# Kernel tuning notes

Hardware: AMD Instinct MI355X
Metric: run time of the kernel (lower is better)

## Reference

```python
import jax, jax.numpy as jnp
import numpy as np

N_DIM = 144           # 9 * patch_size(16)
NUM_CODES = 50257


def setup_inputs() -> dict:
    key = jax.random.key(0)
    k1, k2 = jax.random.split(key)
    z = jax.random.normal(k1, (4, 1024, N_DIM), dtype=jnp.float32)
    # embedding initialized uniform(-1/K, 1/K) as in the torch module
    emb = jax.random.uniform(k2, (NUM_CODES, N_DIM), dtype=jnp.float32,
                             minval=-1.0 / NUM_CODES, maxval=1.0 / NUM_CODES)
    return {"z": z, "emb": emb, "pkeep": 0}


def reference(z, emb, pkeep):
    # flatten to [N, D]
    zf = z.reshape(-1, N_DIM)
    # squared euclidean distances: ||z||^2 + ||e||^2 - 2 z e^T  -> [N, K]
    d = (jnp.sum(zf * zf, axis=1, keepdims=True)
         + jnp.sum(emb * emb, axis=1)
         - 2.0 * jnp.matmul(zf, emb.T))
    min_encoding_indices = jnp.argmin(d, axis=1)          # [N] int
    z_q = emb[min_encoding_indices].reshape(z.shape)      # gather + reshape
    loss = jnp.mean((z_q - z) ** 2)
    # pkeep == 0 in this configuration -> random-replacement branch skipped
    return (z_q, min_encoding_indices, loss)
```

## Files before the change

kernel.cpp:

```cpp
#include <hip/hip_runtime.h>
#include <math.h>

#define D        144
#define KCODES   50257
#define NROWS    4096
#define NS       16
#define CHUNK    3142
#define NT       50
#define NTSW     52
#define CAP      512
#define MARGIN   6.0e-5f
#define ZQ_OFF   0
#define IDX_OFF  589824
#define LOSS_OFF 593920

typedef short bf16x8 __attribute__((ext_vector_type(8)));
typedef float f32x4  __attribute__((ext_vector_type(4)));

#define EHSW_SZ  ((size_t)NS * NTSW * 4 * 5 * 64 * 16)
#define CNT_OFF  EHSW_SZ
#define RMX_OFF  (CNT_OFF + (size_t)NROWS * 4)
#define LIST_OFF (RMX_OFF + (size_t)NROWS * 4)
#define LROW_OFF (LIST_OFF + (size_t)NROWS * CAP * 4)
#define WS_NEED  (LROW_OFF + (size_t)NROWS * 4)

static __device__ __forceinline__ unsigned short f2bf(float x) {
    unsigned int u = __float_as_uint(x);
    u += 0x7fffu + ((u >> 16) & 1u);
    return (unsigned short)(u >> 16);
}
static __device__ __forceinline__ unsigned fkey(float f) {
    unsigned u = __float_as_uint(f);
    return (u & 0x80000000u) ? ~u : (u | 0x80000000u);
}
static __device__ __forceinline__ float fkey_inv(unsigned k) {
    unsigned u = (k & 0x80000000u) ? (k ^ 0x80000000u) : ~k;
    return __uint_as_float(u);
}

__global__ void prep_emb_kernel(const float* __restrict__ emb,
                                unsigned short* __restrict__ EHsw,
                                int* __restrict__ cnt, unsigned* __restrict__ rmx) {
    const int idx = blockIdx.x * 256 + threadIdx.x;
    if (idx < NROWS) { cnt[idx] = 0; rmx[idx] = 0u; }
    if (idx >= NS * NTSW * 4 * 5 * 64) return;
    const int lane = idx & 63;
    int r = idx >> 6;
    const int ks = r % 5;  r /= 5;
    const int w  = r % 4;  r /= 4;
    const int t  = r % NTSW;
    const int sp = r / NTSW;
    const int n  = lane & 15, q = lane >> 4;
    const int code = sp * CHUNK + t * 64 + w * 16 + n;
    const int k0   = ks * 32 + q * 8;
    unsigned short h[8];
    if (code < KCODES && k0 < D) {
        const float4 f0 = *(const float4*)(emb + (size_t)code * D + k0);
        const float4 f1 = *(const float4*)(emb + (size_t)code * D + k0 + 4);
        const float f[8] = {f0.x, f0.y, f0.z, f0.w, f1.x, f1.y, f1.z, f1.w};
        #pragma unroll
        for (int j = 0; j < 8; ++j) h[j] = f2bf(f[j]);
    } else {
        #pragma unroll
        for (int j = 0; j < 8; ++j) h[j] = 0;
    }
    *(uint4*)(EHsw + (size_t)idx * 8) = *(const uint4*)h;
}

#define LOAD_A_FRAGS(zptr)                                                     \
    bf16x8 Ah[4][5];                                                           \
    _Pragma("unroll")                                                          \
    for (int rt = 0; rt < 4; ++rt) {                                           \
        const float* zr = (zptr) + (size_t)(row0 + rt * 16 + n) * D;           \
        _Pragma("unroll")                                                      \
        for (int ks = 0; ks < 5; ++ks) {                                       \
            const int k0 = ks * 32 + q * 8;                                    \
            bf16x8 h;                                                          \
            if (k0 < D) {                                                      \
                const float4 f0 = *(const float4*)(zr + k0);                   \
                const float4 f1 = *(const float4*)(zr + k0 + 4);               \
                const float f[8] = {f0.x, f0.y, f0.z, f0.w,                    \
                                    f1.x, f1.y, f1.z, f1.w};                   \
                _Pragma("unroll")                                              \
                for (int j = 0; j < 8; ++j) h[j] = (short)f2bf(f[j]);          \
            } else {                                                           \
                _Pragma("unroll")                                              \
                for (int j = 0; j < 8; ++j) h[j] = 0;                          \
            }                                                                  \
            Ah[rt][ks] = h;                                                    \
        }                                                                      \
    }

#define LOAD_B(buf, ptr)                                                       \
    _Pragma("unroll")                                                          \
    for (int ks = 0; ks < 5; ++ks)                                             \
        buf[ks] = *(const bf16x8*)((ptr) + (size_t)ks * 1024);

#define MFMA_TILE(buf)                                                         \
    _Pragma("unroll")                                                          \
    for (int rt = 0; rt < 4; ++rt) {                                           \
        acc[rt][0]=0.f; acc[rt][1]=0.f; acc[rt][2]=0.f; acc[rt][3]=0.f;        \
    }                                                                          \
    _Pragma("unroll")                                                          \
    for (int ks = 0; ks < 5; ++ks)                                             \
        _Pragma("unroll")                                                      \
        for (int rt = 0; rt < 4; ++rt)                                         \
            acc[rt] = __builtin_amdgcn_mfma_f32_16x16x32_bf16(                 \
                Ah[rt][ks], buf[ks], acc[rt], 0, 0, 0);

#define CONSUME_MAX                                                            \
    _Pragma("unroll")                                                          \
    for (int rt = 0; rt < 4; ++rt)                                             \
        _Pragma("unroll")                                                      \
        for (int r = 0; r < 4; ++r)                                            \
            ml[rt*4 + r] = fmaxf(ml[rt*4 + r], acc[rt][r]);

#define CONSUME_SEL                                                            \
    _Pragma("unroll")                                                          \
    for (int rt = 0; rt < 4; ++rt)                                             \
        _Pragma("unroll")                                                      \
        for (int r = 0; r < 4; ++r) {                                          \
            const float vm = 2.0f * acc[rt][r];                                \
            if (vm >= thr[rt*4 + r] && code < KCODES) {                        \
                const int row = row0 + rt * 16 + q * 4 + r;                    \
                const int pos = atomicAdd(&cnt[row], 1);                       \
                if (pos < CAP) list[(size_t)row * CAP + pos] = code;           \
            }                                                                  \
        }                                                                      \
    code += 64;

#define TS 20480

__global__ __launch_bounds__(256, 2)
void vq_max_kernel(const float* __restrict__ z,
                   const char* __restrict__ EHsw,
                   unsigned* __restrict__ rmx) {
    const int tid  = threadIdx.x;
    const int w    = tid >> 6;
    const int lane = tid & 63;
    const int n    = lane & 15;
    const int q    = lane >> 4;
    const int sp   = blockIdx.x;
    const int row0 = blockIdx.y * 64;

    LOAD_A_FRAGS(z)

    float ml[16];
    #pragma unroll
    for (int i = 0; i < 16; ++i) ml[i] = -INFINITY;

    const char* pB = EHsw + ((size_t)(sp * NTSW) * 4 + w) * 5120 + lane * 16;

    bf16x8 b0[5], b1[5], b2[5], b3[5];
    f32x4 acc[4];
    LOAD_B(b0, pB)
    LOAD_B(b1, pB + TS)
    LOAD_B(b2, pB + 2 * TS)
    LOAD_B(b3, pB + 3 * TS)
    for (int i = 0; i < 12; ++i) {
        MFMA_TILE(b0) CONSUME_MAX LOAD_B(b0, pB + 4 * TS)
        MFMA_TILE(b1) CONSUME_MAX LOAD_B(b1, pB + 5 * TS)
        MFMA_TILE(b2) CONSUME_MAX LOAD_B(b2, pB + 6 * TS)
        MFMA_TILE(b3) CONSUME_MAX LOAD_B(b3, pB + 7 * TS)
        pB += 4 * TS;
    }
    MFMA_TILE(b0) CONSUME_MAX
    MFMA_TILE(b1) CONSUME_MAX

    __shared__ float wmax[4][64];
    #pragma unroll
    for (int i = 0; i < 16; ++i) {
        float v = ml[i];
        v = fmaxf(v, __shfl_xor(v, 1, 64));
        v = fmaxf(v, __shfl_xor(v, 2, 64));
        v = fmaxf(v, __shfl_xor(v, 4, 64));
        v = fmaxf(v, __shfl_xor(v, 8, 64));
        if (n == 0) wmax[w][(i >> 2) * 16 + q * 4 + (i & 3)] = v;
    }
    __syncthreads();
    if (tid < 64) {
        const float m = fmaxf(fmaxf(wmax[0][tid], wmax[1][tid]),
                              fmaxf(wmax[2][tid], wmax[3][tid])) * 2.0f;
        atomicMax(&rmx[row0 + tid], fkey(m));
    }
}

__global__ __launch_bounds__(256, 2)
void vq_select_kernel(const float* __restrict__ z,
                      const char* __restrict__ EHsw,
                      const unsigned* __restrict__ rmx,
                      int* __restrict__ cnt, int* __restrict__ list) {
    const int tid  = threadIdx.x;
    const int w    = tid >> 6;
    const int lane = tid & 63;
    const int n    = lane & 15;
    const int q    = lane >> 4;
    const int sp   = blockIdx.x;
    const int row0 = blockIdx.y * 64;

    LOAD_A_FRAGS(z)

    float thr[16];
    #pragma unroll
    for (int i = 0; i < 16; ++i) {
        const int row = row0 + (i >> 2) * 16 + q * 4 + (i & 3);
        thr[i] = fkey_inv(rmx[row]) - MARGIN;
    }

    const char* pB = EHsw + ((size_t)(sp * NTSW) * 4 + w) * 5120 + lane * 16;
    int code = sp * CHUNK + w * 16 + n;

    bf16x8 b0[5], b1[5], b2[5], b3[5];
    f32x4 acc[4];
    LOAD_B(b0, pB)
    LOAD_B(b1, pB + TS)
    LOAD_B(b2, pB + 2 * TS)
    LOAD_B(b3, pB + 3 * TS)
    for (int i = 0; i < 12; ++i) {
        MFMA_TILE(b0) CONSUME_SEL LOAD_B(b0, pB + 4 * TS)
        MFMA_TILE(b1) CONSUME_SEL LOAD_B(b1, pB + 5 * TS)
        MFMA_TILE(b2) CONSUME_SEL LOAD_B(b2, pB + 6 * TS)
        MFMA_TILE(b3) CONSUME_SEL LOAD_B(b3, pB + 7 * TS)
        pB += 4 * TS;
    }
    MFMA_TILE(b0) CONSUME_SEL
    MFMA_TILE(b1) CONSUME_SEL
}

__global__ void vq_phaseC_kernel(const float* __restrict__ z,
                                 const float* __restrict__ emb,
                                 const int* __restrict__ cnt,
                                 const int* __restrict__ list,
                                 float* __restrict__ out,
                                 float* __restrict__ lrow) {
    const int r   = blockIdx.x;
    const int tid = threadIdx.x;
    const int lane = tid & 63, wid = tid >> 6;
    __shared__ float zs[D];
    __shared__ float As_;
    __shared__ float bd_s[4]; __shared__ int bi_s[4];
    __shared__ int   bc_s;
    __shared__ float ls_s[4];

    if (tid < D) zs[tid] = z[(size_t)r * D + tid];
    __syncthreads();
    if (tid == 0) {
        float s = 0.f;
        for (int k = 0; k < D; ++k) s = fmaf(zs[k], zs[k], s);
        As_ = s;
    }
    __syncthreads();
    const float A = As_;

    const int nc   = cnt[r];
    const bool full = (nc <= 0) || (nc > CAP);
    const int count = full ? KCODES : nc;

    float bd = INFINITY; int bi = 0x7fffffff;
    for (int i = tid; i < count; i += 256) {
        const int c = full ? i : list[(size_t)r * CAP + i];
        const float4* e4 = (const float4*)(emb + (size_t)c * D);
        float acc = 0.f;
        #pragma unroll
        for (int j = 0; j < 36; ++j) {
            const float4 e = e4[j];
            acc = fmaf(zs[4*j],   e.x, acc);
            acc = fmaf(zs[4*j+1], e.y, acc);
            acc = fmaf(zs[4*j+2], e.z, acc);
            acc = fmaf(zs[4*j+3], e.w, acc);
        }
        const float m2 = 2.0f * acc;
        const float d  = A - m2;
        if (d < bd || (d == bd && c < bi)) { bd = d; bi = c; }
    }
    #pragma unroll
    for (int m = 1; m < 64; m <<= 1) {
        const float od = __shfl_xor(bd, m, 64);
        const int   oi = __shfl_xor(bi, m, 64);
        if (od < bd || (od == bd && oi < bi)) { bd = od; bi = oi; }
    }
    if (lane == 0) { bd_s[wid] = bd; bi_s[wid] = bi; }
    __syncthreads();
    if (tid == 0) {
        float fbd = bd_s[0]; int fbi = bi_s[0];
        for (int k = 1; k < 4; ++k) {
            if (bd_s[k] < fbd || (bd_s[k] == fbd && bi_s[k] < fbi)) { fbd = bd_s[k]; fbi = bi_s[k]; }
        }
        bc_s = fbi;
        out[IDX_OFF + r] = (float)fbi;
    }
    __syncthreads();
    const int bc = bc_s;

    float ls = 0.f;
    if (tid < D) {
        const float e = emb[(size_t)bc * D + tid];
        out[(size_t)r * D + tid] = e;
        const float dl = e - zs[tid];
        ls = dl * dl;
    }
    #pragma unroll
    for (int m = 1; m < 64; m <<= 1) ls += __shfl_xor(ls, m, 64);
    if (lane == 0) ls_s[wid] = ls;
    __syncthreads();
    if (tid == 0) lrow[r] = ls_s[0] + ls_s[1] + ls_s[2] + ls_s[3];
}

__global__ void vq_loss_kernel(const float* __restrict__ lrow, float* __restrict__ out) {
    __shared__ float sm[256];
    const int tid = threadIdx.x;
    float s = 0.f;
    for (int i = tid; i < NROWS; i += 256) s += lrow[i];
    sm[tid] = s; __syncthreads();
    for (int st = 128; st > 0; st >>= 1) {
        if (tid < st) sm[tid] += sm[tid + st];
        __syncthreads();
    }
    if (tid == 0) out[LOSS_OFF] = sm[0] / 589824.0f;
}

#define BM 64
#define BN 64
#define LDP 68
__global__ __launch_bounds__(256, 2)
void vq_argmin_fb(const float* __restrict__ z, const float* __restrict__ emb,
                  float* __restrict__ pd, int* __restrict__ pi) {
    __shared__ float zsm[D][LDP];
    __shared__ float esm[D][LDP];
    __shared__ float Asm[BM];
    const int tid = threadIdx.x;
    const int row0 = blockIdx.x * BM;
    const int sp = blockIdx.y;
    const int c0 = sp * CHUNK;
    const int c1 = (c0 + CHUNK < KCODES) ? (c0 + CHUNK) : KCODES;
    {
        const int r = tid >> 2, p = tid & 3;
        const float4* src = (const float4*)(z + (size_t)(row0 + r) * D);
        #pragma unroll
        for (int i = 0; i < 9; ++i) {
            const int j4 = p + 4 * i;
            const float4 v = src[j4];
            zsm[4*j4+0][r] = v.x; zsm[4*j4+1][r] = v.y;
            zsm[4*j4+2][r] = v.z; zsm[4*j4+3][r] = v.w;
        }
    }
    __syncthreads();
    if (tid < BM) {
        float s = 0.f;
        for (int k = 0; k < D; ++k) { const float t = zsm[k][tid]; s = fmaf(t, t, s); }
        Asm[tid] = s;
    }
    __syncthreads();
    const int tx = tid & 15, ty = tid >> 4;
    float Arow[4];
    #pragma unroll
    for (int i = 0; i < 4; ++i) Arow[i] = Asm[ty*4 + i];
    float bestd[4]; int besti[4];
    #pragma unroll
    for (int i = 0; i < 4; ++i) { bestd[i] = INFINITY; besti[i] = 0x7fffffff; }
    const int ntiles = (c1 - c0 + BN - 1) / BN;
    for (int t = 0; t < ntiles; ++t) {
        const int cb = c0 + t * BN;
        __syncthreads();
        {
            const int cl = tid >> 2, p = tid & 3;
            int crow = cb + cl; if (crow >= KCODES) crow = KCODES - 1;
            const float4* src = (const float4*)(emb + (size_t)crow * D);
            #pragma unroll
            for (int i = 0; i < 9; ++i) {
                const int j4 = p + 4 * i;
                const float4 v = src[j4];
                esm[4*j4+0][cl] = v.x; esm[4*j4+1][cl] = v.y;
                esm[4*j4+2][cl] = v.z; esm[4*j4+3][cl] = v.w;
            }
        }
        __syncthreads();
        float acc[4][4];
        #pragma unroll
        for (int i = 0; i < 4; ++i)
            #pragma unroll
            for (int j = 0; j < 4; ++j) acc[i][j] = 0.f;
        #pragma unroll 4
        for (int k = 0; k < D; ++k) {
            const float4 a = *(const float4*)&zsm[k][ty*4];
            const float4 b = *(const float4*)&esm[k][tx*4];
            acc[0][0]=fmaf(a.x,b.x,acc[0][0]); acc[0][1]=fmaf(a.x,b.y,acc[0][1]);
            acc[0][2]=fmaf(a.x,b.z,acc[0][2]); acc[0][3]=fmaf(a.x,b.w,acc[0][3]);
            acc[1][0]=fmaf(a.y,b.x,acc[1][0]); acc[1][1]=fmaf(a.y,b.y,acc[1][1]);
            acc[1][2]=fmaf(a.y,b.z,acc[1][2]); acc[1][3]=fmaf(a.y,b.w,acc[1][3]);
            acc[2][0]=fmaf(a.z,b.x,acc[2][0]); acc[2][1]=fmaf(a.z,b.y,acc[2][1]);
            acc[2][2]=fmaf(a.z,b.z,acc[2][2]); acc[2][3]=fmaf(a.z,b.w,acc[2][3]);
            acc[3][0]=fmaf(a.w,b.x,acc[3][0]); acc[3][1]=fmaf(a.w,b.y,acc[3][1]);
            acc[3][2]=fmaf(a.w,b.z,acc[3][2]); acc[3][3]=fmaf(a.w,b.w,acc[3][3]);
        }
        #pragma unroll
        for (int j = 0; j < 4; ++j) {
            const int code = cb + tx*4 + j;
            if (code < c1) {
                #pragma unroll
                for (int i = 0; i < 4; ++i) {
                    const float m2 = 2.0f * acc[i][j];
                    const float d  = Arow[i] - m2;
                    if (d < bestd[i] || (d == bestd[i] && code < besti[i])) {
                        bestd[i] = d; besti[i] = code;
                    }
                }
            }
        }
    }
    #pragma unroll
    for (int i = 0; i < 4; ++i) {
        float d = bestd[i]; int idx = besti[i];
        #pragma unroll
        for (int m = 1; m < 16; m <<= 1) {
            const float od = __shfl_xor(d, m, 64);
            const int   oi = __shfl_xor(idx, m, 64);
            if (od < d || (od == d && oi < idx)) { d = od; idx = oi; }
        }
        if (tx == 0) {
            const int r = row0 + ty*4 + i;
            pd[(size_t)sp * NROWS + r] = d;
            pi[(size_t)sp * NROWS + r] = idx;
        }
    }
}

__global__ void vq_finalize_fb(const float* __restrict__ z, const float* __restrict__ emb,
                               const float* __restrict__ pd, const int* __restrict__ pi,
                               float* __restrict__ out, float* __restrict__ lrow) {
    const int r = blockIdx.x * blockDim.x + threadIdx.x;
    if (r >= NROWS) return;
    float bd = INFINITY; int bi = 0x7fffffff;
    for (int s = 0; s < NS; ++s) {
        const float d = pd[(size_t)s * NROWS + r];
        const int  ix = pi[(size_t)s * NROWS + r];
        if (d < bd || (d == bd && ix < bi)) { bd = d; bi = ix; }
    }
    out[IDX_OFF + r] = (float)bi;
    const float4* e4 = (const float4*)(emb + (size_t)bi * D);
    const float4* z4 = (const float4*)(z + (size_t)r * D);
    float4* o4 = (float4*)(out + (size_t)r * D);
    float ls = 0.f;
    #pragma unroll
    for (int j = 0; j < 36; ++j) {
        const float4 e = e4[j], zz = z4[j];
        o4[j] = e;
        const float dx = e.x - zz.x, dy = e.y - zz.y;
        const float dz_ = e.z - zz.z, dw = e.w - zz.w;
        ls += dx*dx + dy*dy + dz_*dz_ + dw*dw;
    }
    lrow[r] = ls;
}

extern "C" void kernel_launch(void* const* d_in, const int* in_sizes, int n_in,
                              void* d_out, int out_size, void* d_ws, size_t ws_size,
                              hipStream_t stream) {
    const float* z   = (const float*)d_in[0];
    const float* emb = (const float*)d_in[1];
    float* out = (float*)d_out;

    if (ws_size >= WS_NEED) {
        unsigned short* EHsw = (unsigned short*)d_ws;
        int*      cnt  = (int*)((char*)d_ws + CNT_OFF);
        unsigned* rmx  = (unsigned*)((char*)d_ws + RMX_OFF);
        int*      list = (int*)((char*)d_ws + LIST_OFF);
        float*    lrow = (float*)((char*)d_ws + LROW_OFF);

        prep_emb_kernel<<<(NS * NTSW * 4 * 5 * 64) / 256, 256, 0, stream>>>(emb, EHsw, cnt, rmx);
        dim3 gs(NS, 64);
        vq_max_kernel<<<gs, 256, 0, stream>>>(z, (const char*)EHsw, rmx);
        vq_select_kernel<<<gs, 256, 0, stream>>>(z, (const char*)EHsw, rmx, cnt, list);
        vq_phaseC_kernel<<<NROWS, 256, 0, stream>>>(z, emb, cnt, list, out, lrow);
        vq_loss_kernel<<<1, 256, 0, stream>>>(lrow, out);
    } else {
        float* pd   = (float*)d_ws;
        int*   pi   = (int*)((char*)d_ws + (size_t)NS * NROWS * 4);
        float* lrow = (float*)((char*)d_ws + (size_t)NS * NROWS * 8);
        dim3 g1(64, NS);
        vq_argmin_fb<<<g1, 256, 0, stream>>>(z, emb, pd, pi);
        vq_finalize_fb<<<16, 256, 0, stream>>>(z, emb, pd, pi, out, lrow);
        vq_loss_kernel<<<1, 256, 0, stream>>>(lrow, out);
    }
}
```

Measured before the change: 282.4 us.

## Double code splits, pre-swizzle z to bf16, warp-skip selection, per-warp exact rescoring

Splits the codebook into 32 chunks instead of 16, giving twice as many blocks for the max and select passes. A new prep kernel converts z to bf16 in MFMA fragment order once, so those passes no longer re-convert z in every block. The select pass now checks all candidates per wave with __any before issuing atomics, and compares against a pre-halved threshold. The exact rescoring kernel assigns one candidate per wave, reduces with shuffles, and computes the norm with a warp reduction. The cost is an extra kernel launch and more per-block prologue work relative to the shorter inner loop.

Result: slower. 427.4 us (+51.4%).

```diff
diff --git a/kernel.cpp b/kernel.cpp
--- a/kernel.cpp
+++ b/kernel.cpp
@@ -4,21 +4,24 @@
 #define D        144
 #define KCODES   50257
 #define NROWS    4096
-#define NS       16
-#define CHUNK    3142
-#define NT       50
-#define NTSW     52
+#define NS       32
+#define CHUNK    1571
+#define NT       25
+#define NTSW     29
 #define CAP      512
 #define MARGIN   6.0e-5f
 #define ZQ_OFF   0
 #define IDX_OFF  589824
 #define LOSS_OFF 593920
+#define TS       20480
 
 typedef short bf16x8 __attribute__((ext_vector_type(8)));
 typedef float f32x4  __attribute__((ext_vector_type(4)));
 
-#define EHSW_SZ  ((size_t)NS * NTSW * 4 * 5 * 64 * 16)
-#define CNT_OFF  EHSW_SZ
+#define EHSW_SZ  ((size_t)NS * NTSW * TS)
+#define ZSW_OFF  EHSW_SZ
+#define ZSW_SZ   ((size_t)64 * 4 * 5 * 64 * 16)
+#define CNT_OFF  (ZSW_OFF + ZSW_SZ)
 #define RMX_OFF  (CNT_OFF + (size_t)NROWS * 4)
 #define LIST_OFF (RMX_OFF + (size_t)NROWS * 4)
 #define LROW_OFF (LIST_OFF + (size_t)NROWS * CAP * 4)
@@ -39,11 +42,8 @@
 }
 
 __global__ void prep_emb_kernel(const float* __restrict__ emb,
-                                unsigned short* __restrict__ EHsw,
-                                int* __restrict__ cnt, unsigned* __restrict__ rmx) {
+                                unsigned short* __restrict__ EHsw) {
     const int idx = blockIdx.x * 256 + threadIdx.x;
-    if (idx < NROWS) { cnt[idx] = 0; rmx[idx] = 0u; }
-    if (idx >= NS * NTSW * 4 * 5 * 64) return;
     const int lane = idx & 63;
     int r = idx >> 6;
     const int ks = r % 5;  r /= 5;
@@ -67,29 +67,41 @@
     *(uint4*)(EHsw + (size_t)idx * 8) = *(const uint4*)h;
 }
 
-#define LOAD_A_FRAGS(zptr)                                                     \
+__global__ void prep_z_kernel(const float* __restrict__ z,
+                              unsigned short* __restrict__ ZSW,
+                              int* __restrict__ cnt, unsigned* __restrict__ rmx) {
+    const int idx = blockIdx.x * 256 + threadIdx.x;
+    if (idx < NROWS) { cnt[idx] = 0; rmx[idx] = 0u; }
+    const int lane = idx & 63;
+    int r = idx >> 6;
+    const int ks = r % 5;  r /= 5;
+    const int rt = r % 4;
+    const int rb = r / 4;
+    const int n  = lane & 15, q = lane >> 4;
+    const int row = rb * 64 + rt * 16 + n;
+    const int k0  = ks * 32 + q * 8;
+    unsigned short h[8];
+    if (k0 < D) {
+        const float4 f0 = *(const float4*)(z + (size_t)row * D + k0);
+        const float4 f1 = *(const float4*)(z + (size_t)row * D + k0 + 4);
+        const float f[8] = {f0.x, f0.y, f0.z, f0.w, f1.x, f1.y, f1.z, f1.w};
+        #pragma unroll
+        for (int j = 0; j < 8; ++j) h[j] = f2bf(f[j]);
+    } else {
+        #pragma unroll
+        for (int j = 0; j < 8; ++j) h[j] = 0;
+    }
+    *(uint4*)(ZSW + (size_t)idx * 8) = *(const uint4*)h;
+}
+
+#define LOAD_A_SW(zsw)                                                         \
     bf16x8 Ah[4][5];                                                           \
     _Pragma("unroll")                                                          \
-    for (int rt = 0; rt < 4; ++rt) {                                           \
-        const float* zr = (zptr) + (size_t)(row0 + rt * 16 + n) * D;           \
+    for (int rt = 0; rt < 4; ++rt)                                             \
         _Pragma("unroll")                                                      \
-        for (int ks = 0; ks < 5; ++ks) {                                       \
-            const int k0 = ks * 32 + q * 8;                                    \
-            bf16x8 h;                                                          \
-            if (k0 < D) {                                                      \
-                const float4 f0 = *(const float4*)(zr + k0);                   \
-                const float4 f1 = *(const float4*)(zr + k0 + 4);               \
-                const float f[8] = {f0.x, f0.y, f0.z, f0.w,                    \
-                                    f1.x, f1.y, f1.z, f1.w};                   \
-                _Pragma("unroll")                                              \
-                for (int j = 0; j < 8; ++j) h[j] = (short)f2bf(f[j]);          \
-            } else {                                                           \
-                _Pragma("unroll")                                              \
-                for (int j = 0; j < 8; ++j) h[j] = 0;                          \
-            }                                                                  \
-            Ah[rt][ks] = h;                                                    \
-        }                                                                      \
-    }
+        for (int ks = 0; ks < 5; ++ks)                                         \
+            Ah[rt][ks] = *(const bf16x8*)((zsw) +                              \
+                (size_t)((((rb * 4 + rt) * 5 + ks) * 64 + lane)) * 16);
 
 #define LOAD_B(buf, ptr)                                                       \
     _Pragma("unroll")                                                          \
@@ -116,23 +128,29 @@
             ml[rt*4 + r] = fmaxf(ml[rt*4 + r], acc[rt][r]);
 
 #define CONSUME_SEL                                                            \
-    _Pragma("unroll")                                                          \
-    for (int rt = 0; rt < 4; ++rt)                                             \
+    {                                                                          \
+        bool anyl = false;                                                     \
         _Pragma("unroll")                                                      \
-        for (int r = 0; r < 4; ++r) {                                          \
-            const float vm = 2.0f * acc[rt][r];                                \
-            if (vm >= thr[rt*4 + r] && code < KCODES) {                        \
-                const int row = row0 + rt * 16 + q * 4 + r;                    \
-                const int pos = atomicAdd(&cnt[row], 1);                       \
-                if (pos < CAP) list[(size_t)row * CAP + pos] = code;           \
-            }                                                                  \
+        for (int rt = 0; rt < 4; ++rt)                                         \
+            _Pragma("unroll")                                                  \
+            for (int r = 0; r < 4; ++r)                                        \
+                anyl |= (acc[rt][r] >= thr2[rt*4 + r]);                        \
+        if (__any(anyl)) {                                                     \
+            _Pragma("unroll")                                                  \
+            for (int rt = 0; rt < 4; ++rt)                                     \
+                _Pragma("unroll")                                              \
+                for (int r = 0; r < 4; ++r)                                    \
+                    if (acc[rt][r] >= thr2[rt*4 + r] && code < KCODES) {       \
+                        const int row = row0 + rt * 16 + q * 4 + r;            \
+                        const int pos = atomicAdd(&cnt[row], 1);               \
+                        if (pos < CAP) list[(size_t)row * CAP + pos] = code;   \
+                    }                                                          \
         }                                                                      \
-    code += 64;
-
-#define TS 20480
+        code += 64;                                                            \
+    }
 
 __global__ __launch_bounds__(256, 2)
-void vq_max_kernel(const float* __restrict__ z,
+void vq_max_kernel(const char* __restrict__ ZSW,
                    const char* __restrict__ EHsw,
                    unsigned* __restrict__ rmx) {
     const int tid  = threadIdx.x;
@@ -141,9 +159,10 @@
     const int n    = lane & 15;
     const int q    = lane >> 4;
     const int sp   = blockIdx.x;
-    const int row0 = blockIdx.y * 64;
-
-    LOAD_A_FRAGS(z)
+    const int rb   = blockIdx.y;
+    const int row0 = rb * 64;
+
+    LOAD_A_SW(ZSW)
 
     float ml[16];
     #pragma unroll
@@ -157,7 +176,7 @@
     LOAD_B(b1, pB + TS)
     LOAD_B(b2, pB + 2 * TS)
     LOAD_B(b3, pB + 3 * TS)
-    for (int i = 0; i < 12; ++i) {
+    for (int i = 0; i < 6; ++i) {
         MFMA_TILE(b0) CONSUME_MAX LOAD_B(b0, pB + 4 * TS)
         MFMA_TILE(b1) CONSUME_MAX LOAD_B(b1, pB + 5 * TS)
         MFMA_TILE(b2) CONSUME_MAX LOAD_B(b2, pB + 6 * TS)
@@ -165,7 +184,6 @@
         pB += 4 * TS;
     }
     MFMA_TILE(b0) CONSUME_MAX
-    MFMA_TILE(b1) CONSUME_MAX
 
     __shared__ float wmax[4][64];
     #pragma unroll
@@ -186,7 +204,7 @@
 }
 
 __global__ __launch_bounds__(256, 2)
-void vq_select_kernel(const float* __restrict__ z,
+void vq_select_kernel(const char* __restrict__ ZSW,
                       const char* __restrict__ EHsw,
                       const unsigned* __restrict__ rmx,
                       int* __restrict__ cnt, int* __restrict__ list) {
@@ -196,15 +214,16 @@
     const int n    = lane & 15;
     const int q    = lane >> 4;
     const int sp   = blockIdx.x;
-    const int row0 = blockIdx.y * 64;
-
-    LOAD_A_FRAGS(z)
-
-    float thr[16];
+    const int rb   = blockIdx.y;
+    const int row0 = rb * 64;
+
+    LOAD_A_SW(ZSW)
+
+    float thr2[16];
     #pragma unroll
     for (int i = 0; i < 16; ++i) {
         const int row = row0 + (i >> 2) * 16 + q * 4 + (i & 3);
-        thr[i] = fkey_inv(rmx[row]) - MARGIN;
+        thr2[i] = (fkey_inv(rmx[row]) - MARGIN) * 0.5f;
     }
 
     const char* pB = EHsw + ((size_t)(sp * NTSW) * 4 + w) * 5120 + lane * 16;
@@ -216,7 +235,7 @@
     LOAD_B(b1, pB + TS)
     LOAD_B(b2, pB + 2 * TS)
     LOAD_B(b3, pB + 3 * TS)
-    for (int i = 0; i < 12; ++i) {
+    for (int i = 0; i < 6; ++i) {
         MFMA_TILE(b0) CONSUME_SEL LOAD_B(b0, pB + 4 * TS)
         MFMA_TILE(b1) CONSUME_SEL LOAD_B(b1, pB + 5 * TS)
         MFMA_TILE(b2) CONSUME_SEL LOAD_B(b2, pB + 6 * TS)
@@ -224,7 +243,6 @@
         pB += 4 * TS;
     }
     MFMA_TILE(b0) CONSUME_SEL
-    MFMA_TILE(b1) CONSUME_SEL
 }
 
 __global__ void vq_phaseC_kernel(const float* __restrict__ z,
@@ -233,77 +251,64 @@
                                  const int* __restrict__ list,
                                  float* __restrict__ out,
                                  float* __restrict__ lrow) {
-    const int r   = blockIdx.x;
-    const int tid = threadIdx.x;
+    const int r    = blockIdx.x;
+    const int tid  = threadIdx.x;
     const int lane = tid & 63, wid = tid >> 6;
-    __shared__ float zs[D];
-    __shared__ float As_;
+    __shared__ float4 zs4[36];
     __shared__ float bd_s[4]; __shared__ int bi_s[4];
     __shared__ int   bc_s;
-    __shared__ float ls_s[4];
-
-    if (tid < D) zs[tid] = z[(size_t)r * D + tid];
-    __syncthreads();
-    if (tid == 0) {
-        float s = 0.f;
-        for (int k = 0; k < D; ++k) s = fmaf(zs[k], zs[k], s);
-        As_ = s;
-    }
-    __syncthreads();
-    const float A = As_;
+
+    if (tid < 36) zs4[tid] = ((const float4*)(z + (size_t)r * D))[tid];
+    __syncthreads();
+
+    float4 z4 = {0.f, 0.f, 0.f, 0.f};
+    if (lane < 36) z4 = zs4[lane];
+
+    float a = z4.x*z4.x + z4.y*z4.y + z4.z*z4.z + z4.w*z4.w;
+    #pragma unroll
+    for (int m = 1; m < 64; m <<= 1) a += __shfl_xor(a, m, 64);
+    const float A = a;
 
     const int nc   = cnt[r];
     const bool full = (nc <= 0) || (nc > CAP);
     const int count = full ? KCODES : nc;
 
     float bd = INFINITY; int bi = 0x7fffffff;
-    for (int i = tid; i < count; i += 256) {
-        const int c = full ? i : list[(size_t)r * CAP + i];
-        const float4* e4 = (const float4*)(emb + (size_t)c * D);
-        float acc = 0.f;
-        #pragma unroll
-        for (int j = 0; j < 36; ++j) {
-            const float4 e = e4[j];
-            acc = fmaf(zs[4*j],   e.x, acc);
-            acc = fmaf(zs[4*j+1], e.y, acc);
-            acc = fmaf(zs[4*j+2], e.z, acc);
-            acc = fmaf(zs[4*j+3], e.w, acc);
-        }
-        const float m2 = 2.0f * acc;
-        const float d  = A - m2;
+    for (int ci = wid; ci < count; ci += 4) {
+        const int c = full ? ci : list[(size_t)r * CAP + ci];
+        float4 e4 = {0.f, 0.f, 0.f, 0.f};
+        if (lane < 36) e4 = ((const float4*)(emb + (size_t)c * D))[lane];
+        float p = z4.x*e4.x + z4.y*e4.y + z4.z*e4.z + z4.w*e4.w;
+        #pragma unroll
+        for (int m = 1; m < 64; m <<= 1) p += __shfl_xor(p, m, 64);
+        const float d = A - 2.0f * p;
         if (d < bd || (d == bd && c < bi)) { bd = d; bi = c; }
-    }
-    #pragma unroll
-    for (int m = 1; m < 64; m <<= 1) {
-        const float od = __shfl_xor(bd, m, 64);
-        const int   oi = __shfl_xor(bi, m, 64);
-        if (od < bd || (od == bd && oi < bi)) { bd = od; bi = oi; }
     }
     if (lane == 0) { bd_s[wid] = bd; bi_s[wid] = bi; }
     __syncthreads();
     if (tid == 0) {
         float fbd = bd_s[0]; int fbi = bi_s[0];
-        for (int k = 1; k < 4; ++k) {
+        for (int k = 1; k < 4; ++k)
             if (bd_s[k] < fbd || (bd_s[k] == fbd && bi_s[k] < fbi)) { fbd = bd_s[k]; fbi = bi_s[k]; }
-        }
         bc_s = fbi;
         out[IDX_OFF + r] = (float)fbi;
     }
     __syncthreads();
     const int bc = bc_s;
 
-    float ls = 0.f;
-    if (tid < D) {
-        const float e = emb[(size_t)bc * D + tid];
-        out[(size_t)r * D + tid] = e;
-        const float dl = e - zs[tid];
-        ls = dl * dl;
-    }
-    #pragma unroll
-    for (int m = 1; m < 64; m <<= 1) ls += __shfl_xor(ls, m, 64);
-    if (lane == 0) ls_s[wid] = ls;
-    __syncthreads();
-    if (tid == 0) lrow[r] = ls_s[0] + ls_s[1] + ls_s[2] + ls_s[3];
+    if (wid == 0) {
+        float ls = 0.f;
+        if (lane < 36) {
+            const float4 e4 = ((const float4*)(emb + (size_t)bc * D))[lane];
+            ((float4*)(out + (size_t)r * D))[lane] = e4;
+            const float dx = e4.x - z4.x, dy = e4.y - z4.y;
+            const float dz_ = e4.z - z4.z, dw = e4.w - z4.w;
+            ls = dx*dx + dy*dy + dz_*dz_ + dw*dw;
+        }
+        #pragma unroll
+        for (int m = 1; m < 64; m <<= 1) ls += __shfl_xor(ls, m, 64);
+        if (lane == 0) lrow[r] = ls;
+    }
 }
 
 __global__ void vq_loss_kernel(const float* __restrict__ lrow, float* __restrict__ out) {
@@ -319,6 +324,7 @@
     if (tid == 0) out[LOSS_OFF] = sm[0] / 589824.0f;
 }
 
+#define FCHUNK 3142
 #define BM 64
 #define BN 64
 #define LDP 68
@@ -331,8 +337,8 @@
     const int tid = threadIdx.x;
     const int row0 = blockIdx.x * BM;
     const int sp = blockIdx.y;
-    const int c0 = sp * CHUNK;
-    const int c1 = (c0 + CHUNK < KCODES) ? (c0 + CHUNK) : KCODES;
+    const int c0 = sp * FCHUNK;
+    const int c1 = (c0 + FCHUNK < KCODES) ? (c0 + FCHUNK) : KCODES;
     {
         const int r = tid >> 2, p = tid & 3;
         const float4* src = (const float4*)(z + (size_t)(row0 + r) * D);
@@ -431,7 +437,7 @@
     const int r = blockIdx.x * blockDim.x + threadIdx.x;
     if (r >= NROWS) return;
     float bd = INFINITY; int bi = 0x7fffffff;
-    for (int s = 0; s < NS; ++s) {
+    for (int s = 0; s < 16; ++s) {
         const float d = pd[(size_t)s * NROWS + r];
         const int  ix = pi[(size_t)s * NROWS + r];
         if (d < bd || (d == bd && ix < bi)) { bd = d; bi = ix; }
@@ -461,22 +467,24 @@
 
     if (ws_size >= WS_NEED) {
         unsigned short* EHsw = (unsigned short*)d_ws;
+        unsigned short* ZSW  = (unsigned short*)((char*)d_ws + ZSW_OFF);
         int*      cnt  = (int*)((char*)d_ws + CNT_OFF);
         unsigned* rmx  = (unsigned*)((char*)d_ws + RMX_OFF);
         int*      list = (int*)((char*)d_ws + LIST_OFF);
         float*    lrow = (float*)((char*)d_ws + LROW_OFF);
 
-        prep_emb_kernel<<<(NS * NTSW * 4 * 5 * 64) / 256, 256, 0, stream>>>(emb, EHsw, cnt, rmx);
+        prep_emb_kernel<<<(NS * NTSW * 4 * 5 * 64) / 256, 256, 0, stream>>>(emb, EHsw);
+        prep_z_kernel<<<(64 * 4 * 5 * 64) / 256, 256, 0, stream>>>(z, ZSW, cnt, rmx);
         dim3 gs(NS, 64);
-        vq_max_kernel<<<gs, 256, 0, stream>>>(z, (const char*)EHsw, rmx);
-        vq_select_kernel<<<gs, 256, 0, stream>>>(z, (const char*)EHsw, rmx, cnt, list);
+        vq_max_kernel<<<gs, 256, 0, stream>>>((const char*)ZSW, (const char*)EHsw, rmx);
+        vq_select_kernel<<<gs, 256, 0, stream>>>((const char*)ZSW, (const char*)EHsw, rmx, cnt, list);
         vq_phaseC_kernel<<<NROWS, 256, 0, stream>>>(z, emb, cnt, list, out, lrow);
         vq_loss_kernel<<<1, 256, 0, stream>>>(lrow, out);
     } else {
         float* pd   = (float*)d_ws;
-        int*   pi   = (int*)((char*)d_ws + (size_t)NS * NROWS * 4);
-        float* lrow = (float*)((char*)d_ws + (size_t)NS * NROWS * 8);
-        dim3 g1(64, NS);
+        int*   pi   = (int*)((char*)d_ws + (size_t)16 * NROWS * 4);
+        float* lrow = (float*)((char*)d_ws + (size_t)16 * NROWS * 8);
+        dim3 g1(64, 16);
         vq_argmin_fb<<<g1, 256, 0, stream>>>(z, emb, pd, pi);
         vq_finalize_fb<<<16, 256, 0, stream>>>(z, emb, pd, pi, out, lrow);
         vq_loss_kernel<<<1, 256, 0, stream>>>(lrow, out);
```
